# Optimization experiments

Hardware: AMD Instinct MI355X
Metric: run time of the kernel (lower is better)

Reference implementation:

```python
import jax, jax.numpy as jnp
import numpy as np

N, C_IN, H, W = 32, 128, 56, 56
C_OUT, KH, KW = 256, 3, 3
STRIDE = (1, 1)
PAD = (1, 1)


def setup_inputs() -> dict:
    key = jax.random.key(0)
    k_x, k_w, k_b = jax.random.split(key, 3)
    x = jax.random.normal(k_x, (N, C_IN, H, W), dtype=jnp.float32)
    # kaiming_uniform-like scale for weight, uniform bias in [-1/sqrt(fan_in), 1/sqrt(fan_in)]
    fan_in = C_IN * KH * KW
    bound_w = float(np.sqrt(6.0 / ((1 + 5.0) * fan_in)))  # kaiming_uniform a=sqrt(5)
    weight = jax.random.uniform(k_w, (C_OUT, C_IN, KH, KW), dtype=jnp.float32,
                                minval=-bound_w, maxval=bound_w)
    bound_b = float(1.0 / np.sqrt(fan_in))
    bias = jax.random.uniform(k_b, (C_OUT,), dtype=jnp.float32,
                              minval=-bound_b, maxval=bound_b)
    return {"x": x, "weight": weight, "bias": bias}


def reference(x, weight, bias):
    # Faithful math of the im2col conv: zero padding (ph,pw)=(1,1), stride 1,
    # groups=1 -> identical to a standard cross-correlation conv2d + bias.
    out = jax.lax.conv_general_dilated(
        x, weight,
        window_strides=STRIDE,
        padding=[(PAD[0], PAD[0]), (PAD[1], PAD[1])],
        dimension_numbers=("NCHW", "OIHW", "NCHW"),
    )
    return out + bias[None, :, None, None]
```

## Files before the change

kernel.cpp:

```cpp
#include <hip/hip_runtime.h>


#define NB   32
#define CIN  128
#define HH   56
#define WWD  56
#define COUT 256
#define HWP  3136
#define KTOT 1152
#define MTOT 100352

typedef __bf16 bf16x8 __attribute__((ext_vector_type(8)));
typedef float  f32x4  __attribute__((ext_vector_type(4)));
typedef unsigned short u16;
typedef u16 u16x4 __attribute__((ext_vector_type(4)));
typedef u16 u16x8 __attribute__((ext_vector_type(8)));

__device__ __forceinline__ u16 f2b(float f) {
  unsigned u = __float_as_uint(f);
  u += 0x7fffu + ((u >> 16) & 1u);
  return (u16)(u >> 16);
}

__device__ __forceinline__ void load_lds16(const void* g, void* l) {
  __builtin_amdgcn_global_load_lds(
      (const __attribute__((address_space(1))) unsigned int*)g,
      (__attribute__((address_space(3))) unsigned int*)l, 16, 0, 0);
}

__global__ __launch_bounds__(256) void k_transpose_x(const float* __restrict__ x,
                                                     u16* __restrict__ xt) {
  __shared__ u16 tile[64][68];
  const int n  = blockIdx.z;
  const int p0 = blockIdx.x * 64;
  const int c0 = blockIdx.y * 64;
  const int t  = threadIdx.x;

  const float* xp = x + (size_t)n * CIN * HWP + (size_t)c0 * HWP + p0;
  const int pl = (t & 15) * 4;
  const int cr = t >> 4;
#pragma unroll
  for (int j = 0; j < 4; ++j) {
    int c = cr + j * 16;
    f32x4 v = *(const f32x4*)&xp[(size_t)c * HWP + pl];
    u16x4 h;
    h[0] = f2b(v[0]); h[1] = f2b(v[1]); h[2] = f2b(v[2]); h[3] = f2b(v[3]);
    *(u16x4*)&tile[c][pl] = h;
  }
  __syncthreads();
  u16* xo = xt + (size_t)n * HWP * CIN + (size_t)p0 * CIN + c0;
  const int ch = (t & 7) * 8;
  const int pr = t >> 3;
#pragma unroll
  for (int j = 0; j < 2; ++j) {
    int p = pr + j * 32;
    u16x8 o;
#pragma unroll
    for (int i = 0; i < 8; ++i) o[i] = tile[ch + i][p];
    *(u16x8*)&xo[(size_t)p * CIN + ch] = o;
  }
}

__global__ __launch_bounds__(256) void k_transform_w(const float* __restrict__ w,
                                                     u16* __restrict__ Wt,
                                                     u16* __restrict__ zb) {
  int o = blockIdx.x * 256 + threadIdx.x;
  if (o < COUT * KTOT) {
    int co  = o / KTOT;
    int rem = o - co * KTOT;
    int kk  = rem >> 7;
    int ci  = rem & 127;
    int kh  = kk / 3;
    int kw  = kk - kh * 3;
    Wt[o] = f2b(w[(((size_t)co * CIN + ci) * 3 + kh) * 3 + kw]);
  }
  if (blockIdx.x == 0 && threadIdx.x < 128) zb[threadIdx.x] = 0;
}

__global__ __launch_bounds__(256, 4) void k_conv_gemm(
    const u16* __restrict__ xt, const u16* __restrict__ Wt,
    const u16* __restrict__ zb, const float* __restrict__ bias,
    float* __restrict__ out) {
  __shared__ u16 lW[128 * 64];
  __shared__ u16 lX[128 * 64];

  const int tid  = threadIdx.x;
  const int wave = tid >> 6;
  const int lane = tid & 63;
  const int m0   = blockIdx.x * 128;
  const int co0  = blockIdx.y * 128;

  const int wrow = (wave >> 1) * 64;
  const int wcol = (wave & 1) * 64;

  const int rsub = lane >> 3;
  const int pso  = (((lane & 7) ^ rsub)) * 8;

  int soh[4], sow[4], sbase[4];
#pragma unroll
  for (int c = 0; c < 4; ++c) {
    int chunk = wave * 4 + c;
    int m = m0 + chunk * 8 + rsub;
    int n = m / HWP;
    int s = m - n * HWP;
    int oh = s / WWD;
    int ow = s - oh * WWD;
    soh[c] = oh; sow[c] = ow;
    sbase[c] = n * HWP + oh * WWD + ow;
  }

  f32x4 acc[4][4];
#pragma unroll
  for (int i = 0; i < 4; ++i)
#pragma unroll
    for (int j = 0; j < 4; ++j) acc[i][j] = (f32x4){0.f, 0.f, 0.f, 0.f};

  const int r  = lane & 15;
  const int q  = lane >> 4;
  const int r7 = r & 7;

  for (int kt = 0; kt < 18; ++kt) {
    const int ksp = kt >> 1;
    const int kh  = ksp / 3;
    const int kw  = ksp - kh * 3;
    const int ci0 = (kt & 1) << 6;
    const int kg  = kt << 6;

    __syncthreads();
#pragma unroll
    for (int c = 0; c < 4; ++c) {
      int rowW = wave * 32 + c * 8;
      const u16* g = Wt + (size_t)(co0 + rowW + rsub) * KTOT + kg + pso;
      load_lds16(g, &lW[rowW * 64]);
    }
#pragma unroll
    for (int c = 0; c < 4; ++c) {
      int ih = soh[c] + kh - 1;
      int iw = sow[c] + kw - 1;
      bool valid = ((unsigned)ih < HH) && ((unsigned)iw < WWD);
      const u16* g = valid
          ? xt + (size_t)(sbase[c] + (kh - 1) * WWD + (kw - 1)) * CIN + ci0 + pso
          : zb + pso;
      load_lds16(g, &lX[(wave * 32 + c * 8) * 64]);
    }
    __syncthreads();

#pragma unroll
    for (int kk = 0; kk < 2; ++kk) {
      bf16x8 a[4], b[4];
      const int sw = ((kk * 4 + q) ^ r7) * 8;
#pragma unroll
      for (int ti = 0; ti < 4; ++ti)
        a[ti] = *(const bf16x8*)(&lW[(wrow + ti * 16 + r) * 64 + sw]);
#pragma unroll
      for (int tj = 0; tj < 4; ++tj)
        b[tj] = *(const bf16x8*)(&lX[(wcol + tj * 16 + r) * 64 + sw]);
#pragma unroll
      for (int ti = 0; ti < 4; ++ti)
#pragma unroll
        for (int tj = 0; tj < 4; ++tj)
          acc[ti][tj] =
              __builtin_amdgcn_mfma_f32_16x16x32_bf16(a[ti], b[tj], acc[ti][tj], 0, 0, 0);
    }
  }

#pragma unroll
  for (int tj = 0; tj < 4; ++tj) {
    int m = m0 + wcol + tj * 16 + r;
    int n = m / HWP;
    int s = m - n * HWP;
#pragma unroll
    for (int ti = 0; ti < 4; ++ti) {
      f32x4 v = acc[ti][tj];
#pragma unroll
      for (int e = 0; e < 4; ++e) {
        int co = co0 + wrow + ti * 16 + q * 4 + e;
        out[((size_t)n * COUT + co) * HWP + s] = v[e] + bias[co];
      }
    }
  }
}

extern "C" void kernel_launch(void* const* d_in, const int* in_sizes, int n_in,
                              void* d_out, int out_size, void* d_ws, size_t ws_size,
                              hipStream_t stream) {
  const float* x    = (const float*)d_in[0];
  const float* w    = (const float*)d_in[1];
  const float* bias = (const float*)d_in[2];
  float* out        = (float*)d_out;

  u16* xt = (u16*)d_ws;
  u16* Wt = xt + (size_t)NB * HWP * CIN;
  u16* zb = Wt + (size_t)COUT * KTOT;

  k_transform_w<<<dim3(1152), dim3(256), 0, stream>>>(w, Wt, zb);
  k_transpose_x<<<dim3(49, 2, 32), dim3(256), 0, stream>>>(x, xt);
  k_conv_gemm<<<dim3(784, 2), dim3(256), 0, stream>>>(xt, Wt, zb, bias, out);
}
```

Measured before the change: 210.2 us.

## Pad input layout and software-pipeline a 256x256-tile conv GEMM with multi-buffered LDS

```diff
diff --git a/kernel.cpp b/kernel.cpp
--- a/kernel.cpp
+++ b/kernel.cpp
@@ -8,7 +8,8 @@
 #define COUT 256
 #define HWP  3136
 #define KTOT 1152
-#define MTOT 100352
+#define HP   58
+#define XTN  (HP*HP*CIN)
 
 typedef __bf16 bf16x8 __attribute__((ext_vector_type(8)));
 typedef float  f32x4  __attribute__((ext_vector_type(4)));
@@ -22,7 +23,7 @@
   return (u16)(u >> 16);
 }
 
-__device__ __forceinline__ void load_lds16(const void* g, void* l) {
+__device__ __forceinline__ void load_lds16(const u16* g, u16* l) {
   __builtin_amdgcn_global_load_lds(
       (const __attribute__((address_space(1))) unsigned int*)g,
       (__attribute__((address_space(3))) unsigned int*)l, 16, 0, 0);
@@ -48,22 +49,25 @@
     *(u16x4*)&tile[c][pl] = h;
   }
   __syncthreads();
-  u16* xo = xt + (size_t)n * HWP * CIN + (size_t)p0 * CIN + c0;
+  u16* xb = xt + (size_t)n * XTN + c0;
   const int ch = (t & 7) * 8;
   const int pr = t >> 3;
 #pragma unroll
   for (int j = 0; j < 2; ++j) {
-    int p = pr + j * 32;
+    int p  = pr + j * 32;
+    int s  = p0 + p;
+    int oh = s / WWD;
+    int ow = s - oh * WWD;
     u16x8 o;
 #pragma unroll
     for (int i = 0; i < 8; ++i) o[i] = tile[ch + i][p];
-    *(u16x8*)&xo[(size_t)p * CIN + ch] = o;
+    *(u16x8*)&xb[((size_t)(oh + 1) * HP + (ow + 1)) * CIN + ch] = o;
   }
 }
 
 __global__ __launch_bounds__(256) void k_transform_w(const float* __restrict__ w,
                                                      u16* __restrict__ Wt,
-                                                     u16* __restrict__ zb) {
+                                                     u16* __restrict__ xt) {
   int o = blockIdx.x * 256 + threadIdx.x;
   if (o < COUT * KTOT) {
     int co  = o / KTOT;
@@ -74,109 +78,163 @@
     int kw  = kk - kh * 3;
     Wt[o] = f2b(w[(((size_t)co * CIN + ci) * 3 + kh) * 3 + kw]);
   }
-  if (blockIdx.x == 0 && threadIdx.x < 128) zb[threadIdx.x] = 0;
-}
-
-__global__ __launch_bounds__(256, 4) void k_conv_gemm(
+#pragma unroll
+  for (int j = 0; j < 4; ++j) {
+    unsigned e = (unsigned)o + j * 294912u;
+    if (e < 933888u) {
+      unsigned n  = e / 29184u;
+      unsigned rm = e - n * 29184u;
+      unsigned bp = rm >> 7;
+      unsigned ch = rm & 127u;
+      unsigned ih, iw;
+      if (bp < 58u)       { ih = 0;  iw = bp; }
+      else if (bp < 116u) { ih = 57; iw = bp - 58u; }
+      else { unsigned c2 = bp - 116u; ih = 1u + (c2 >> 1); iw = (c2 & 1u) ? 57u : 0u; }
+      xt[(((size_t)n * HP + ih) * HP + iw) * CIN + ch] = (u16)0;
+    }
+  }
+}
+
+
+#define RD_A(qm_) do { _Pragma("unroll") for (int kk = 0; kk < 2; ++kk) \
+    { _Pragma("unroll") for (int ti = 0; ti < 4; ++ti) \
+      a[kk][ti] = *(const bf16x8*)&lds[eA + (wm*128 + (qm_)*64 + ti*16 + r)*64 \
+                                        + (((kk*4 + q) ^ r7))*8]; } } while (0)
+
+#define RD_B(qn_) do { _Pragma("unroll") for (int kk = 0; kk < 2; ++kk) \
+    { _Pragma("unroll") for (int tj = 0; tj < 2; ++tj) \
+      b[kk][tj] = *(const bf16x8*)&lds[eB + (wn*64 + (qn_)*32 + tj*16 + r)*64 \
+                                        + (((kk*4 + q) ^ r7))*8]; } } while (0)
+
+#define MM(qm_, qn_) do { _Pragma("unroll") for (int kk = 0; kk < 2; ++kk) \
+    { _Pragma("unroll") for (int ti = 0; ti < 4; ++ti) \
+      { _Pragma("unroll") for (int tj = 0; tj < 2; ++tj) \
+        acc[(qm_)*4 + ti][(qn_)*2 + tj] = __builtin_amdgcn_mfma_f32_16x16x32_bf16( \
+            a[kk][ti], b[kk][tj], acc[(qm_)*4 + ti][(qn_)*2 + tj], 0, 0, 0); } } } while (0)
+
+__global__ __launch_bounds__(512, 2) void k_conv_gemm(
     const u16* __restrict__ xt, const u16* __restrict__ Wt,
-    const u16* __restrict__ zb, const float* __restrict__ bias,
-    float* __restrict__ out) {
-  __shared__ u16 lW[128 * 64];
-  __shared__ u16 lX[128 * 64];
-
+    const float* __restrict__ bias, float* __restrict__ out) {
+  extern __shared__ u16 lds[];
   const int tid  = threadIdx.x;
   const int wave = tid >> 6;
   const int lane = tid & 63;
-  const int m0   = blockIdx.x * 128;
-  const int co0  = blockIdx.y * 128;
-
-  const int wrow = (wave >> 1) * 64;
-  const int wcol = (wave & 1) * 64;
-
-  const int rsub = lane >> 3;
-  const int pso  = (((lane & 7) ^ rsub)) * 8;
-
-  int soh[4], sow[4], sbase[4];
-#pragma unroll
-  for (int c = 0; c < 4; ++c) {
-    int chunk = wave * 4 + c;
-    int m = m0 + chunk * 8 + rsub;
-    int n = m / HWP;
-    int s = m - n * HWP;
-    int oh = s / WWD;
-    int ow = s - oh * WWD;
-    soh[c] = oh; sow[c] = ow;
-    sbase[c] = n * HWP + oh * WWD + ow;
-  }
-
-  f32x4 acc[4][4];
-#pragma unroll
-  for (int i = 0; i < 4; ++i)
-#pragma unroll
-    for (int j = 0; j < 4; ++j) acc[i][j] = (f32x4){0.f, 0.f, 0.f, 0.f};
-
+  const int m0   = blockIdx.x * 256;
+
+  const int wm = wave >> 2;
+  const int wn = wave & 3;
   const int r  = lane & 15;
   const int q  = lane >> 4;
   const int r7 = r & 7;
 
+  const int rsub = lane >> 3;
+  const int ps8  = ((lane & 7) ^ rsub) * 8;
+
+  int pbA[4], pbB[4], ldo[4];
+#pragma unroll
+  for (int j = 0; j < 4; ++j) {
+    const int rowb = wave * 8 + j * 64;
+    const int m  = m0 + rowb + rsub;
+    const int n  = m / HWP;
+    const int s  = m - n * HWP;
+    const int oh = s / WWD;
+    const int ow = s - oh * WWD;
+    pbA[j] = ((n * HP + oh) * HP + ow) * CIN + ps8;
+    pbB[j] = (rowb + rsub) * KTOT + ps8;
+    ldo[j] = rowb * 64;
+  }
+  float bias_r[4];
+#pragma unroll
+  for (int tj = 0; tj < 4; ++tj) bias_r[tj] = bias[wn * 64 + tj * 16 + r];
+
+  f32x4 acc[8][4];
+#pragma unroll
+  for (int i = 0; i < 8; ++i)
+#pragma unroll
+    for (int jj = 0; jj < 4; ++jj) acc[i][jj] = (f32x4){0.f, 0.f, 0.f, 0.f};
+
+#pragma unroll
+  for (int j = 0; j < 4; ++j) load_lds16(Wt + pbB[j], &lds[49152 + ldo[j]]);
+#pragma unroll
+  for (int j = 0; j < 4; ++j) load_lds16(xt + pbA[j], &lds[0 + ldo[j]]);
+#pragma unroll
+  for (int j = 0; j < 4; ++j) load_lds16(xt + pbA[j] + 64, &lds[16384 + ldo[j]]);
+  asm volatile("s_waitcnt vmcnt(4)" ::: "memory");
+  __builtin_amdgcn_s_barrier();
+
+  bf16x8 a[2][4], b[2][2];
+  int bA = 0, bB = 0;
+
+#pragma unroll 1
   for (int kt = 0; kt < 18; ++kt) {
-    const int ksp = kt >> 1;
-    const int kh  = ksp / 3;
-    const int kw  = ksp - kh * 3;
-    const int ci0 = (kt & 1) << 6;
-    const int kg  = kt << 6;
-
-    __syncthreads();
-#pragma unroll
-    for (int c = 0; c < 4; ++c) {
-      int rowW = wave * 32 + c * 8;
-      const u16* g = Wt + (size_t)(co0 + rowW + rsub) * KTOT + kg + pso;
-      load_lds16(g, &lW[rowW * 64]);
-    }
-#pragma unroll
-    for (int c = 0; c < 4; ++c) {
-      int ih = soh[c] + kh - 1;
-      int iw = sow[c] + kw - 1;
-      bool valid = ((unsigned)ih < HH) && ((unsigned)iw < WWD);
-      const u16* g = valid
-          ? xt + (size_t)(sbase[c] + (kh - 1) * WWD + (kw - 1)) * CIN + ci0 + pso
-          : zb + pso;
-      load_lds16(g, &lX[(wave * 32 + c * 8) * 64]);
-    }
-    __syncthreads();
-
-#pragma unroll
-    for (int kk = 0; kk < 2; ++kk) {
-      bf16x8 a[4], b[4];
-      const int sw = ((kk * 4 + q) ^ r7) * 8;
-#pragma unroll
-      for (int ti = 0; ti < 4; ++ti)
-        a[ti] = *(const bf16x8*)(&lW[(wrow + ti * 16 + r) * 64 + sw]);
-#pragma unroll
-      for (int tj = 0; tj < 4; ++tj)
-        b[tj] = *(const bf16x8*)(&lX[(wcol + tj * 16 + r) * 64 + sw]);
-#pragma unroll
-      for (int ti = 0; ti < 4; ++ti)
-#pragma unroll
-        for (int tj = 0; tj < 4; ++tj)
-          acc[ti][tj] =
-              __builtin_amdgcn_mfma_f32_16x16x32_bf16(a[ti], b[tj], acc[ti][tj], 0, 0, 0);
-    }
-  }
-
-#pragma unroll
-  for (int tj = 0; tj < 4; ++tj) {
-    int m = m0 + wcol + tj * 16 + r;
-    int n = m / HWP;
-    int s = m - n * HWP;
-#pragma unroll
-    for (int ti = 0; ti < 4; ++ti) {
+    const int eA  = bA * 16384;
+    const int eB  = 49152 + bB * 16384;
+    const int sAo = (bA == 0) ? 32768 : (bA - 1) * 16384;
+    const int sBo = 49152 + ((bB ^ 1) * 16384);
+    const int koffB = (kt + 1) * 64;
+    const int kt2  = kt + 2;
+    const int ksp2 = kt2 >> 1;
+    const int kh2  = (ksp2 >= 6) ? 2 : ((ksp2 >= 3) ? 1 : 0);
+    const int kw2  = ksp2 - kh2 * 3;
+    const int UA   = (kh2 * HP + kw2) * CIN + ((kt2 & 1) << 6);
+    const bool doB = (kt < 17);
+    const bool doA = (kt < 16);
+
+    RD_A(0); RD_B(0);
+    if (doB) { load_lds16(Wt + pbB[0] + koffB, &lds[sBo + ldo[0]]);
+               load_lds16(Wt + pbB[1] + koffB, &lds[sBo + ldo[1]]); }
+    __builtin_amdgcn_s_barrier();
+    __builtin_amdgcn_s_setprio(1);
+    MM(0, 0);
+    __builtin_amdgcn_s_setprio(0);
+    __builtin_amdgcn_s_barrier();
+
+    RD_B(1);
+    if (doB) { load_lds16(Wt + pbB[2] + koffB, &lds[sBo + ldo[2]]);
+               load_lds16(Wt + pbB[3] + koffB, &lds[sBo + ldo[3]]); }
+    __builtin_amdgcn_s_barrier();
+    __builtin_amdgcn_s_setprio(1);
+    MM(0, 1);
+    __builtin_amdgcn_s_setprio(0);
+    __builtin_amdgcn_s_barrier();
+
+    RD_A(1);
+    if (doA) { load_lds16(xt + pbA[0] + UA, &lds[sAo + ldo[0]]);
+               load_lds16(xt + pbA[1] + UA, &lds[sAo + ldo[1]]); }
+    __builtin_amdgcn_s_barrier();
+    __builtin_amdgcn_s_setprio(1);
+    MM(1, 1);
+    __builtin_amdgcn_s_setprio(0);
+    __builtin_amdgcn_s_barrier();
+
+    RD_B(0);
+    if (doA) { load_lds16(xt + pbA[2] + UA, &lds[sAo + ldo[2]]);
+               load_lds16(xt + pbA[3] + UA, &lds[sAo + ldo[3]]); }
+    if (kt < 16) { asm volatile("s_waitcnt vmcnt(4)" ::: "memory"); }
+    else         { asm volatile("s_waitcnt vmcnt(0)" ::: "memory"); }
+    __builtin_amdgcn_s_barrier();
+    __builtin_amdgcn_s_setprio(1);
+    MM(1, 0);
+    __builtin_amdgcn_s_setprio(0);
+    __builtin_amdgcn_s_barrier();
+
+    bA = (bA == 2) ? 0 : bA + 1;
+    bB ^= 1;
+  }
+
+#pragma unroll
+  for (int ti = 0; ti < 8; ++ti) {
+    const int m4 = m0 + wm * 128 + ti * 16 + q * 4;
+    const int n  = m4 / HWP;
+    const int s  = m4 - n * HWP;
+    float* op = out + (size_t)n * COUT * HWP + s;
+#pragma unroll
+    for (int tj = 0; tj < 4; ++tj) {
+      const int co = wn * 64 + tj * 16 + r;
       f32x4 v = acc[ti][tj];
-#pragma unroll
-      for (int e = 0; e < 4; ++e) {
-        int co = co0 + wrow + ti * 16 + q * 4 + e;
-        out[((size_t)n * COUT + co) * HWP + s] = v[e] + bias[co];
-      }
+      const float bv = bias_r[tj];
+      v[0] += bv; v[1] += bv; v[2] += bv; v[3] += bv;
+      *(f32x4*)(op + (size_t)co * HWP) = v;
     }
   }
 }
@@ -190,10 +248,16 @@
   float* out        = (float*)d_out;
 
   u16* xt = (u16*)d_ws;
-  u16* Wt = xt + (size_t)NB * HWP * CIN;
-  u16* zb = Wt + (size_t)COUT * KTOT;
-
-  k_transform_w<<<dim3(1152), dim3(256), 0, stream>>>(w, Wt, zb);
+  u16* Wt = xt + (size_t)NB * XTN;
+
+  static bool attr_done = false;
+  if (!attr_done) {
+    hipFuncSetAttribute(reinterpret_cast<const void*>(k_conv_gemm),
+                        hipFuncAttributeMaxDynamicSharedMemorySize, 163840);
+    attr_done = true;
+  }
+
+  k_transform_w<<<dim3(1152), dim3(256), 0, stream>>>(w, Wt, xt);
   k_transpose_x<<<dim3(49, 2, 32), dim3(256), 0, stream>>>(x, xt);
-  k_conv_gemm<<<dim3(784, 2), dim3(256), 0, stream>>>(xt, Wt, zb, bias, out);
-}
+  k_conv_gemm<<<dim3(392), dim3(512), 163840, stream>>>(xt, Wt, bias, out);
+}
```

New measurement: 219.7 us. 1.05x slower.
